# Performance work log

Measured on AMD Instinct MI355X. Metric: run time of the kernel, lower is better.

Reference implementation:

```python
import jax, jax.numpy as jnp
import numpy as np

EMBED_DIM = 1024
HEADS = 16
DIM_HEAD = 64  # embed_dim // heads
SCALE = DIM_HEAD ** -0.5


def setup_inputs() -> dict:
    key = jax.random.key(0)
    ks = jax.random.split(key, 6)
    x = jax.random.normal(ks[0], (2, 2048, EMBED_DIM), dtype=jnp.float32)
    # qkv_proj: Linear(embed_dim, 3*embed_dim) with bias
    w_qkv = jax.random.normal(ks[1], (EMBED_DIM, 3 * EMBED_DIM), dtype=jnp.float32) * (EMBED_DIM ** -0.5)
    b_qkv = jax.random.normal(ks[2], (3 * EMBED_DIM,), dtype=jnp.float32) * 0.01
    # out_proj: Linear(embed_dim, embed_dim) with bias
    w_out = jax.random.normal(ks[3], (EMBED_DIM, EMBED_DIM), dtype=jnp.float32) * (EMBED_DIM ** -0.5)
    b_out = jax.random.normal(ks[4], (EMBED_DIM,), dtype=jnp.float32) * 0.01
    return {"x": x, "w_qkv": w_qkv, "b_qkv": b_qkv, "w_out": w_out, "b_out": b_out}


def reference(x, w_qkv, b_qkv, w_out, b_out):
    b, s, d = x.shape
    h, dh = HEADS, d // HEADS
    qkv = x @ w_qkv + b_qkv                       # [b, s, 3d]
    qkv = qkv.reshape(b, s, 3, h, dh)
    qkv = jnp.transpose(qkv, (0, 3, 2, 1, 4))     # [b, h, 3, s, dh]
    q, k, v = qkv[:, :, 0], qkv[:, :, 1], qkv[:, :, 2]
    q = q * SCALE
    attn = jnp.einsum("bhqd,bhkd->bhqk", q, k)    # [b, h, s, s]
    attn = jax.nn.softmax(attn.astype(jnp.float32), axis=-1).astype(attn.dtype)
    # attn_dropout p=0 -> identity
    out = jnp.einsum("bhqk,bhkd->bhqd", attn, v)  # [b, h, s, dh]
    out = jnp.transpose(out, (0, 2, 1, 3)).reshape(b, s, d)
    return out @ w_out + b_out
```

## Files before the change

### kernel.cpp

```cpp
#include <hip/hip_runtime.h>

#define EMBED  1024
#define HEADS  16
#define DHEAD  64
#define SEQ    2048
#define BATCH  2
#define NTOK   4096
#define QS2    (0.125f * 1.44269504089f)
#define DEFER_THR 8.0f

typedef unsigned short u16t;
typedef float f32x4 __attribute__((ext_vector_type(4)));
typedef __bf16 bf16x8 __attribute__((ext_vector_type(8)));
typedef u16t u16x8 __attribute__((ext_vector_type(8)));
typedef u16t u16x4 __attribute__((ext_vector_type(4)));
typedef unsigned u32x4 __attribute__((ext_vector_type(4)));

static __device__ __forceinline__ u16t f2bf(float f) {
    unsigned u = __builtin_bit_cast(unsigned, f);
    return (u16t)((u + 0x7fffu + ((u >> 16) & 1u)) >> 16);
}
static __device__ __forceinline__ bf16x8 asbf(u16x8 v) {
    return __builtin_bit_cast(bf16x8, v);
}
static __device__ __forceinline__ f32x4 mfma16(bf16x8 a, bf16x8 b, f32x4 c) {
    return __builtin_amdgcn_mfma_f32_16x16x32_bf16(a, b, c, 0, 0, 0);
}
static __device__ __forceinline__ unsigned cvtpk(float lo, float hi) {
    unsigned r;
    asm("v_cvt_pk_bf16_f32 %0, %1, %2" : "=v"(r) : "v"(lo), "v"(hi));
    return r;
}

typedef const __attribute__((address_space(1))) void* as1cv;
typedef __attribute__((address_space(3))) void* as3v;
static __device__ __forceinline__ void ldsload16(const void* g, void* l) {
    __builtin_amdgcn_global_load_lds((as1cv)g, (as3v)l, 16, 0, 0);
}

__global__ __launch_bounds__(256)
void xcvt(const float* __restrict__ X, u16t* __restrict__ XB)
{
    const size_t i = ((size_t)blockIdx.x * 256 + threadIdx.x) * 8;
    float4 a = *(const float4*)&X[i];
    float4 b = *(const float4*)&X[i + 4];
    u16x8 o;
    o[0] = f2bf(a.x); o[1] = f2bf(a.y); o[2] = f2bf(a.z); o[3] = f2bf(a.w);
    o[4] = f2bf(b.x); o[5] = f2bf(b.y); o[6] = f2bf(b.z); o[7] = f2bf(b.w);
    *(u16x8*)&XB[i] = o;
}

__global__ __launch_bounds__(256)
void wtrans(const float* __restrict__ W, u16t* __restrict__ WT, int K, int N)
{
    __shared__ float L[64][65];
    const int t = threadIdx.x;
    const int k0 = blockIdx.y * 64, n0 = blockIdx.x * 64;
#pragma unroll
    for (int rep = 0; rep < 4; ++rep) {
        const int id = rep * 256 + t;
        const int kk = id >> 4, nc = (id & 15) * 4;
        float4 v = *(const float4*)&W[(size_t)(k0 + kk) * N + n0 + nc];
        L[kk][nc] = v.x; L[kk][nc + 1] = v.y; L[kk][nc + 2] = v.z; L[kk][nc + 3] = v.w;
    }
    __syncthreads();
#pragma unroll
    for (int rep = 0; rep < 2; ++rep) {
        const int id = rep * 256 + t;
        const int n = id >> 3, kc = (id & 7) * 8;
        u16x8 o;
#pragma unroll
        for (int i = 0; i < 8; ++i) o[i] = f2bf(L[kc + i][n]);
        *(u16x8*)&WT[(size_t)(n0 + n) * K + k0 + kc] = o;
    }
}

__global__ __launch_bounds__(256)
void vtrans(const u16t* __restrict__ V, u16t* __restrict__ Vt)
{
    __shared__ u16t L[64][65];
    const int t = threadIdx.x;
    const int bh = blockIdx.y;
    const int s0 = blockIdx.x * 64;
    const u16t* src = V + ((size_t)bh * SEQ + s0) * DHEAD;
#pragma unroll
    for (int rep = 0; rep < 2; ++rep) {
        const int id = rep * 256 + t;
        const int s = id >> 3, dc = (id & 7) * 8;
        u16x8 v = *(const u16x8*)&src[(size_t)s * DHEAD + dc];
#pragma unroll
        for (int i = 0; i < 8; ++i) L[s][dc + i] = v[i];
    }
    __syncthreads();
    u16t* dstb = Vt + (size_t)bh * DHEAD * SEQ + s0;
#pragma unroll
    for (int rep = 0; rep < 2; ++rep) {
        const int id = rep * 256 + t;
        const int d = id >> 3, sc = (id & 7) * 8;
        u16x8 o;
#pragma unroll
        for (int i = 0; i < 8; ++i) o[i] = L[sc + i][d];
        *(u16x8*)&dstb[(size_t)d * SEQ + sc] = o;
    }
}

template <int MODE>
__global__ __launch_bounds__(256)
void gemm_bf16(const u16t* __restrict__ A, const u16t* __restrict__ BT,
               const float* __restrict__ bias, int N,
               float* __restrict__ C0, u16t* __restrict__ Qo,
               u16t* __restrict__ Ko, u16t* __restrict__ Vo)
{
    __shared__ __align__(16) u16t Al[128 * 64];
    __shared__ __align__(16) u16t Bl[128 * 64];
    const int t = threadIdx.x;
    const int lane = t & 63;
    const int g = lane >> 4, l15 = lane & 15;
    const int w = t >> 6, wr = w >> 1, wc = w & 1;
    const int m0 = blockIdx.y * 128, n0 = blockIdx.x * 128;

    const int srow = w * 32;
    const int lrow = lane >> 3;
    const int lcolsw = ((lane & 7) ^ lrow) * 8;

    const int r7 = l15 & 7;

    f32x4 acc[4][4] = {};

    for (int k0 = 0; k0 < EMBED; k0 += 64) {
        __syncthreads();
#pragma unroll
        for (int r_ = 0; r_ < 4; ++r_) {
            const int row_ = srow + r_ * 8;
            ldsload16(&A [(size_t)(m0 + row_ + lrow) * EMBED + k0 + lcolsw], &Al[row_ * 64]);
            ldsload16(&BT[(size_t)(n0 + row_ + lrow) * EMBED + k0 + lcolsw], &Bl[row_ * 64]);
        }
        __syncthreads();
#pragma unroll
        for (int kk = 0; kk < 2; ++kk) {
            bf16x8 av[4], bv[4];
#pragma unroll
            for (int i = 0; i < 4; ++i) {
                const int chA = ((kk * 4 + g) ^ r7) * 8;
                av[i] = asbf(*(const u16x8*)&Al[(wr * 64 + i * 16 + l15) * 64 + chA]);
                bv[i] = asbf(*(const u16x8*)&Bl[(wc * 64 + i * 16 + l15) * 64 + chA]);
            }
#pragma unroll
            for (int i = 0; i < 4; ++i)
#pragma unroll
                for (int j = 0; j < 4; ++j)
                    acc[i][j] = mfma16(av[i], bv[j], acc[i][j]);
        }
    }

#pragma unroll
    for (int i = 0; i < 4; ++i)
#pragma unroll
        for (int j = 0; j < 4; ++j)
#pragma unroll
            for (int r = 0; r < 4; ++r) {
                const int row = m0 + wr * 64 + i * 16 + g * 4 + r;
                const int col = n0 + wc * 64 + j * 16 + l15;
                float v = acc[i][j][r] + bias[col];
                if (MODE == 0) {
                    C0[(size_t)row * N + col] = v;
                } else {
                    const int tt = col >> 10, c1 = col & 1023;
                    const int h = c1 >> 6, d = c1 & 63;
                    const int b = row >> 11, s = row & 2047;
                    if (tt == 0) v *= QS2;
                    u16t* dst = (tt == 0) ? Qo : (tt == 1 ? Ko : Vo);
                    dst[(((size_t)b * HEADS + h) * SEQ + s) * DHEAD + d] = f2bf(v);
                }
            }
}

__global__ __launch_bounds__(256)
void attn_mfma(const u16t* __restrict__ Q, const u16t* __restrict__ K,
               const u16t* __restrict__ Vt, u16t* __restrict__ AO)
{
    __shared__ __align__(16) u16t Kl[64][72];
    __shared__ __align__(16) u16t Vl[64][72];
    const int t = threadIdx.x;
    const int lane = t & 63, wq = t >> 6;
    const int g = lane >> 4, l15 = lane & 15;
    const int bh = blockIdx.y;
    const int q0 = blockIdx.x * 128;
    const int b = bh >> 4, h = bh & 15;

    const u16t* qbase = Q + ((size_t)bh * SEQ + q0 + wq * 32) * DHEAD;
    bf16x8 qf[2][2];
#pragma unroll
    for (int qh = 0; qh < 2; ++qh)
#pragma unroll
        for (int kk = 0; kk < 2; ++kk)
            qf[qh][kk] = asbf(*(const u16x8*)&qbase[(size_t)(qh * 16 + l15) * DHEAD + kk * 32 + g * 8]);

    const int srow = t >> 3, scol = (t & 7) * 8;
    const u16t* Kb = K + (size_t)bh * SEQ * DHEAD;
    const u16t* Vb = Vt + (size_t)bh * DHEAD * SEQ;

    {
        u16x8 k0r[2], v0r[2];
#pragma unroll
        for (int rep = 0; rep < 2; ++rep) {
            const int r = rep * 32 + srow;
            k0r[rep] = *(const u16x8*)&Kb[(size_t)r * DHEAD + scol];
            v0r[rep] = *(const u16x8*)&Vb[(size_t)r * SEQ + scol];
        }
#pragma unroll
        for (int rep = 0; rep < 2; ++rep) {
            const int r = rep * 32 + srow;
            *(u16x8*)&Kl[r][scol] = k0r[rep];
            *(u16x8*)&Vl[r][scol] = v0r[rep];
        }
    }
    __syncthreads();

    f32x4 accO[4][2] = {};
    float mrun[2] = {-1e30f, -1e30f}, lrun[2] = {0.f, 0.f};

    for (int kv0 = 0; kv0 < SEQ; kv0 += 64) {
        const bool more = (kv0 + 64 < SEQ);
        u16x8 kreg[2], vreg[2];
        if (more) {
#pragma unroll
            for (int rep = 0; rep < 2; ++rep) {
                const int r = rep * 32 + srow;
                kreg[rep] = *(const u16x8*)&Kb[(size_t)(kv0 + 64 + r) * DHEAD + scol];
                vreg[rep] = *(const u16x8*)&Vb[(size_t)r * SEQ + kv0 + 64 + scol];
            }
        }

        f32x4 s4[4][2] = {};
#pragma unroll
        for (int kk = 0; kk < 2; ++kk)
#pragma unroll
            for (int mf = 0; mf < 4; ++mf) {
                bf16x8 a = asbf(*(const u16x8*)&Kl[mf * 16 + l15][kk * 32 + g * 8]);
                s4[mf][0] = mfma16(a, qf[0][kk], s4[mf][0]);
                s4[mf][1] = mfma16(a, qf[1][kk], s4[mf][1]);
            }

        float mt[2];
#pragma unroll
        for (int qh = 0; qh < 2; ++qh) {
            float m = s4[0][qh][0];
#pragma unroll
            for (int mf = 0; mf < 4; ++mf)
#pragma unroll
                for (int r = 0; r < 4; ++r) m = fmaxf(m, s4[mf][qh][r]);
            m = fmaxf(m, __shfl_xor(m, 16));
            m = fmaxf(m, __shfl_xor(m, 32));
            mt[qh] = m;
        }
        const bool skip =
            __all((mt[0] - mrun[0] <= DEFER_THR) && (mt[1] - mrun[1] <= DEFER_THR)) != 0;
        float mnew[2];
#pragma unroll
        for (int qh = 0; qh < 2; ++qh)
            mnew[qh] = skip ? mrun[qh] : fmaxf(mrun[qh], mt[qh]);

        float p[4][2][4], rs[2] = {0.f, 0.f};
#pragma unroll
        for (int mf = 0; mf < 4; ++mf)
#pragma unroll
            for (int qh = 0; qh < 2; ++qh)
#pragma unroll
                for (int r = 0; r < 4; ++r) {
                    p[mf][qh][r] = __builtin_amdgcn_exp2f(s4[mf][qh][r] - mnew[qh]);
                    rs[qh] += p[mf][qh][r];
                }
#pragma unroll
        for (int qh = 0; qh < 2; ++qh) {
            rs[qh] += __shfl_xor(rs[qh], 16);
            rs[qh] += __shfl_xor(rs[qh], 32);
        }

        if (skip) {
            lrun[0] += rs[0];
            lrun[1] += rs[1];
        } else {
#pragma unroll
            for (int qh = 0; qh < 2; ++qh) {
                const float alpha = __builtin_amdgcn_exp2f(mrun[qh] - mnew[qh]);
                lrun[qh] = lrun[qh] * alpha + rs[qh];
                mrun[qh] = mnew[qh];
                float al[4];
#pragma unroll
                for (int r = 0; r < 4; ++r) al[r] = __shfl(alpha, g * 4 + r);
#pragma unroll
                for (int nf = 0; nf < 4; ++nf)
#pragma unroll
                    for (int r = 0; r < 4; ++r) accO[nf][qh][r] *= al[r];
            }
        }

        u16x8 pu[2][2];
#pragma unroll
        for (int kk = 0; kk < 2; ++kk)
#pragma unroll
            for (int qh = 0; qh < 2; ++qh) {
                const int a = kk * 2;
                u32x4 pw;
                pw[0] = cvtpk(p[a][qh][0], p[a][qh][1]);
                pw[1] = cvtpk(p[a][qh][2], p[a][qh][3]);
                pw[2] = cvtpk(p[a + 1][qh][0], p[a + 1][qh][1]);
                pw[3] = cvtpk(p[a + 1][qh][2], p[a + 1][qh][3]);
                pu[kk][qh] = __builtin_bit_cast(u16x8, pw);
            }

#pragma unroll
        for (int kk = 0; kk < 2; ++kk)
#pragma unroll
            for (int nf = 0; nf < 4; ++nf) {
                const u16t* vr = &Vl[nf * 16 + l15][0];
                u16x4 lo = *(const u16x4*)&vr[kk * 32 + g * 4];
                u16x4 hi = *(const u16x4*)&vr[kk * 32 + 16 + g * 4];
                u16x8 bb = __builtin_shufflevector(lo, hi, 0, 1, 2, 3, 4, 5, 6, 7);
                accO[nf][0] = mfma16(asbf(pu[kk][0]), asbf(bb), accO[nf][0]);
                accO[nf][1] = mfma16(asbf(pu[kk][1]), asbf(bb), accO[nf][1]);
            }

        __syncthreads();
        if (more) {
#pragma unroll
            for (int rep = 0; rep < 2; ++rep) {
                const int r = rep * 32 + srow;
                *(u16x8*)&Kl[r][scol] = kreg[rep];
                *(u16x8*)&Vl[r][scol] = vreg[rep];
            }
            __syncthreads();
        }
    }

#pragma unroll
    for (int qh = 0; qh < 2; ++qh) {
        const float inv = 1.f / lrun[qh];
        float iv[4];
#pragma unroll
        for (int r = 0; r < 4; ++r) iv[r] = __shfl(inv, g * 4 + r);
#pragma unroll
        for (int nf = 0; nf < 4; ++nf)
#pragma unroll
            for (int r = 0; r < 4; ++r) {
                const int s = q0 + wq * 32 + qh * 16 + g * 4 + r;
                AO[((size_t)b * SEQ + s) * EMBED + h * DHEAD + nf * 16 + l15] =
                    f2bf(accO[nf][qh][r] * iv[r]);
            }
    }
}

extern "C" void kernel_launch(void* const* d_in, const int* in_sizes, int n_in,
                              void* d_out, int out_size, void* d_ws, size_t ws_size,
                              hipStream_t stream)
{
    const float* x     = (const float*)d_in[0];
    const float* w_qkv = (const float*)d_in[1];
    const float* b_qkv = (const float*)d_in[2];
    const float* w_out = (const float*)d_in[3];
    const float* b_out = (const float*)d_in[4];

    u16t* xb  = (u16t*)d_ws;
    u16t* wqt = xb  + (size_t)NTOK * EMBED;
    u16t* wot = wqt + (size_t)3072 * 1024;
    u16t* Qb  = wot + (size_t)1024 * 1024;
    u16t* Kb  = Qb  + (size_t)NTOK * EMBED;
    u16t* Vb  = Kb  + (size_t)NTOK * EMBED;
    u16t* Vtb = Vb  + (size_t)NTOK * EMBED;
    u16t* AOb = Vtb + (size_t)NTOK * EMBED;

    xcvt<<<2048, 256, 0, stream>>>(x, xb);
    wtrans<<<dim3(48, 16), 256, 0, stream>>>(w_qkv, wqt, 1024, 3072);
    wtrans<<<dim3(16, 16), 256, 0, stream>>>(w_out, wot, 1024, 1024);

    gemm_bf16<1><<<dim3(24, 32), 256, 0, stream>>>(xb, wqt, b_qkv, 3072,
                                                   nullptr, Qb, Kb, Vb);
    vtrans<<<dim3(32, 32), 256, 0, stream>>>(Vb, Vtb);
    attn_mfma<<<dim3(16, 32), 256, 0, stream>>>(Qb, Kb, Vtb, AOb);
    gemm_bf16<0><<<dim3(8, 32), 256, 0, stream>>>(AOb, wot, b_out, 1024,
                                                  (float*)d_out, nullptr, nullptr, nullptr);
}
```

Baseline: 225.3 us.

## Double-buffer GEMM LDS staging, shrink out-proj tile, raise MFMA priority in attention

```diff
diff --git a/kernel.cpp b/kernel.cpp
--- a/kernel.cpp
+++ b/kernel.cpp
@@ -104,62 +104,83 @@
     }
 }
 
-template <int MODE>
+template <int MODE, int FM>
 __global__ __launch_bounds__(256)
 void gemm_bf16(const u16t* __restrict__ A, const u16t* __restrict__ BT,
                const float* __restrict__ bias, int N,
                float* __restrict__ C0, u16t* __restrict__ Qo,
                u16t* __restrict__ Ko, u16t* __restrict__ Vo)
 {
-    __shared__ __align__(16) u16t Al[128 * 64];
-    __shared__ __align__(16) u16t Bl[128 * 64];
+    constexpr int BM = FM * 32;
+    __shared__ __align__(16) u16t Al[2][BM * 64];
+    __shared__ __align__(16) u16t Bl[2][128 * 64];
     const int t = threadIdx.x;
     const int lane = t & 63;
     const int g = lane >> 4, l15 = lane & 15;
     const int w = t >> 6, wr = w >> 1, wc = w & 1;
-    const int m0 = blockIdx.y * 128, n0 = blockIdx.x * 128;
-
-    const int srow = w * 32;
+    const int m0 = blockIdx.y * BM, n0 = blockIdx.x * 128;
+
+    const int asrow = w * (FM * 8);
+    const int bsrow = w * 32;
     const int lrow = lane >> 3;
     const int lcolsw = ((lane & 7) ^ lrow) * 8;
 
     const int r7 = l15 & 7;
 
-    f32x4 acc[4][4] = {};
-
+#define GSTAGE(buf, k0)                                                           \
+    {                                                                             \
+        _Pragma("unroll")                                                         \
+        for (int r_ = 0; r_ < FM; ++r_) {                                         \
+            const int row_ = asrow + r_ * 8;                                      \
+            ldsload16(&A[(size_t)(m0 + row_ + lrow) * EMBED + (k0) + lcolsw],     \
+                      &Al[buf][row_ * 64]);                                       \
+        }                                                                         \
+        _Pragma("unroll")                                                         \
+        for (int r_ = 0; r_ < 4; ++r_) {                                          \
+            const int row_ = bsrow + r_ * 8;                                      \
+            ldsload16(&BT[(size_t)(n0 + row_ + lrow) * EMBED + (k0) + lcolsw],    \
+                      &Bl[buf][row_ * 64]);                                       \
+        }                                                                         \
+    }
+
+    f32x4 acc[FM][4] = {};
+
+    GSTAGE(0, 0);
+    __syncthreads();
+
+    int cur = 0;
     for (int k0 = 0; k0 < EMBED; k0 += 64) {
-        __syncthreads();
-#pragma unroll
-        for (int r_ = 0; r_ < 4; ++r_) {
-            const int row_ = srow + r_ * 8;
-            ldsload16(&A [(size_t)(m0 + row_ + lrow) * EMBED + k0 + lcolsw], &Al[row_ * 64]);
-            ldsload16(&BT[(size_t)(n0 + row_ + lrow) * EMBED + k0 + lcolsw], &Bl[row_ * 64]);
-        }
-        __syncthreads();
+        if (k0 + 64 < EMBED) GSTAGE(cur ^ 1, k0 + 64);
+        const u16t* Ab = &Al[cur][0];
+        const u16t* Bb = &Bl[cur][0];
 #pragma unroll
         for (int kk = 0; kk < 2; ++kk) {
-            bf16x8 av[4], bv[4];
-#pragma unroll
-            for (int i = 0; i < 4; ++i) {
-                const int chA = ((kk * 4 + g) ^ r7) * 8;
-                av[i] = asbf(*(const u16x8*)&Al[(wr * 64 + i * 16 + l15) * 64 + chA]);
-                bv[i] = asbf(*(const u16x8*)&Bl[(wc * 64 + i * 16 + l15) * 64 + chA]);
-            }
-#pragma unroll
-            for (int i = 0; i < 4; ++i)
+            const int chA = ((kk * 4 + g) ^ r7) * 8;
+            bf16x8 av[FM], bv[4];
+#pragma unroll
+            for (int i = 0; i < FM; ++i)
+                av[i] = asbf(*(const u16x8*)&Ab[(wr * (FM * 16) + i * 16 + l15) * 64 + chA]);
+#pragma unroll
+            for (int j = 0; j < 4; ++j)
+                bv[j] = asbf(*(const u16x8*)&Bb[(wc * 64 + j * 16 + l15) * 64 + chA]);
+#pragma unroll
+            for (int i = 0; i < FM; ++i)
 #pragma unroll
                 for (int j = 0; j < 4; ++j)
                     acc[i][j] = mfma16(av[i], bv[j], acc[i][j]);
         }
-    }
-
-#pragma unroll
-    for (int i = 0; i < 4; ++i)
+        __syncthreads();
+        cur ^= 1;
+    }
+#undef GSTAGE
+
+#pragma unroll
+    for (int i = 0; i < FM; ++i)
 #pragma unroll
         for (int j = 0; j < 4; ++j)
 #pragma unroll
             for (int r = 0; r < 4; ++r) {
-                const int row = m0 + wr * 64 + i * 16 + g * 4 + r;
+                const int row = m0 + wr * (FM * 16) + i * 16 + g * 4 + r;
                 const int col = n0 + wc * 64 + j * 16 + l15;
                 float v = acc[i][j][r] + bias[col];
                 if (MODE == 0) {
@@ -233,6 +254,7 @@
         }
 
         f32x4 s4[4][2] = {};
+        __builtin_amdgcn_s_setprio(1);
 #pragma unroll
         for (int kk = 0; kk < 2; ++kk)
 #pragma unroll
@@ -241,6 +263,7 @@
                 s4[mf][0] = mfma16(a, qf[0][kk], s4[mf][0]);
                 s4[mf][1] = mfma16(a, qf[1][kk], s4[mf][1]);
             }
+        __builtin_amdgcn_s_setprio(0);
 
         float mt[2];
 #pragma unroll
@@ -310,6 +333,7 @@
                 pu[kk][qh] = __builtin_bit_cast(u16x8, pw);
             }
 
+        __builtin_amdgcn_s_setprio(1);
 #pragma unroll
         for (int kk = 0; kk < 2; ++kk)
 #pragma unroll
@@ -321,6 +345,7 @@
                 accO[nf][0] = mfma16(asbf(pu[kk][0]), asbf(bb), accO[nf][0]);
                 accO[nf][1] = mfma16(asbf(pu[kk][1]), asbf(bb), accO[nf][1]);
             }
+        __builtin_amdgcn_s_setprio(0);
 
         __syncthreads();
         if (more) {
@@ -374,10 +399,10 @@
     wtrans<<<dim3(48, 16), 256, 0, stream>>>(w_qkv, wqt, 1024, 3072);
     wtrans<<<dim3(16, 16), 256, 0, stream>>>(w_out, wot, 1024, 1024);
 
-    gemm_bf16<1><<<dim3(24, 32), 256, 0, stream>>>(xb, wqt, b_qkv, 3072,
-                                                   nullptr, Qb, Kb, Vb);
+    gemm_bf16<1, 4><<<dim3(24, 32), 256, 0, stream>>>(xb, wqt, b_qkv, 3072,
+                                                      nullptr, Qb, Kb, Vb);
     vtrans<<<dim3(32, 32), 256, 0, stream>>>(Vb, Vtb);
     attn_mfma<<<dim3(16, 32), 256, 0, stream>>>(Qb, Kb, Vtb, AOb);
-    gemm_bf16<0><<<dim3(8, 32), 256, 0, stream>>>(AOb, wot, b_out, 1024,
-                                                  (float*)d_out, nullptr, nullptr, nullptr);
-}
+    gemm_bf16<0, 2><<<dim3(8, 64), 256, 0, stream>>>(AOb, wot, b_out, 1024,
+                                                     (float*)d_out, nullptr, nullptr, nullptr);
+}
```

Measured after the change: 217.7 us. 1.03x faster.
